# Kernel optimization log

Measured on AMD Instinct MI355X. Metric: run time of the kernel, lower is better.

The kernel has to match this reference:

```python
import jax, jax.numpy as jnp
import numpy as np

K = 7            # kernel size per spatial dim
HALF = K // 2    # 3
WIN = K * K      # 49


def _rel_dist():
    # matches torch: meshgrid('ij') of arange(k)-k//2, euclidean dist, flattened row-major
    c = np.arange(K, dtype=np.float32) - HALF
    gi, gj = np.meshgrid(c, c, indexing='ij')
    return jnp.asarray(np.sqrt(gi ** 2 + gj ** 2).reshape(-1))


def _unfold2d(t):
    B, H, W, C = t.shape
    p = jnp.pad(t, ((0, 0), (HALF, HALF), (HALF, HALF), (0, 0)))
    wins = [p[:, i:i + H, j:j + W, :] for i in range(K) for j in range(K)]
    return jnp.stack(wins, axis=3)


def setup_inputs() -> dict:
    key = jax.random.key(0)
    k1, k2, k3, k4, k5 = jax.random.split(key, 5)
    B, H, W, C = 4, 64, 64, 128
    x = jax.random.normal(k1, (B, H, W, C), dtype=jnp.float32)
    W_qkv = jax.random.normal(k2, (C, 3 * C), dtype=jnp.float32) * (C ** -0.5)
    # width_proj is zero-initialized in the module; use small random values to exercise the soft mask
    W_width = jax.random.normal(k3, (C, 1), dtype=jnp.float32) * 0.02
    b_width = jax.random.normal(k4, (1,), dtype=jnp.float32) * 0.02
    W_out = jax.random.normal(k5, (C, C), dtype=jnp.float32) * (C ** -0.5)
    return {"x": x, "W_qkv": W_qkv, "W_width": W_width, "b_width": b_width, "W_out": W_out}


def reference(x, W_qkv, W_width, b_width, W_out):
    B, H, W, C = x.shape
    L = H * W
    scale = C ** -0.5
    rel_dist = _rel_dist()
    max_dist = rel_dist.max()

    qkv = x @ W_qkv                              # (B,H,W,3C)
    q, k, v = jnp.split(qkv, 3, axis=-1)
    width = jax.nn.sigmoid(x @ W_width + b_width) * max_dist + 0.5  # (B,H,W,1)

    k_win = _unfold2d(k).reshape(B, L, WIN, C)
    v_win = _unfold2d(v).reshape(B, L, WIN, C)
    q_flat = q.reshape(B, L, C)
    width_flat = width.reshape(B, L, 1)

    scores = jnp.einsum('blc,blwc->blw', q_flat, k_win) * scale
    soft_mask = jax.nn.sigmoid((width_flat - rel_dist) * 5.0)
    scores = scores - (1.0 - soft_mask) * 10000.0
    attn = jax.nn.softmax(scores, axis=-1)
    out = jnp.einsum('blw,blwc->blc', attn, v_win).reshape(B, H, W, C)
    return (out + v) @ W_out
```

## Files before the change

### kernel.cpp

```cpp
#include <hip/hip_runtime.h>

#define C 128
#define NPIX 16384
#define THREE_C 384

typedef unsigned short u16;
typedef unsigned int u32;
typedef short bf16x8 __attribute__((ext_vector_type(8)));
typedef float f32x4 __attribute__((ext_vector_type(4)));

__device__ __forceinline__ float bf2f(u16 h) { return __uint_as_float(((u32)h) << 16); }
__device__ __forceinline__ u16 f2bf(float f) {
    u32 b = __float_as_uint(f);
    b += 0x7FFF + ((b >> 16) & 1);
    return (u16)(b >> 16);
}
__device__ __forceinline__ u32 pack2(float a, float b) {
    return (u32)f2bf(a) | ((u32)f2bf(b) << 16);
}

#define GST 136

__global__ __launch_bounds__(256) void qkv_kernel(const float* __restrict__ x,
                                                  const float* __restrict__ Wqkv,
                                                  const float* __restrict__ Wwidth,
                                                  const float* __restrict__ bwidth,
                                                  const float* __restrict__ Wout,
                                                  u16* __restrict__ qb,
                                                  u16* __restrict__ kb,
                                                  u16* __restrict__ vb,
                                                  float* __restrict__ width_g,
                                                  u16* __restrict__ wot) {
    __shared__ u16 xs[64 * GST];
    __shared__ u16 wt[128 * GST];
    const int task = ((int)(blockIdx.x & 7)) * 96 + ((int)blockIdx.x >> 3);
    const int rb = task / 3;
    const int nb = task % 3;
    const int p0 = rb * 64;
    const int tid = threadIdx.x;
    const int wv = tid >> 6;
    const int l = tid & 63;
    const int l15 = l & 15;
    const int l4 = l >> 4;

#pragma unroll
    for (int t = 0; t < 8; ++t) {
        const int f = tid + t * 256;
        const int kq = f & 31, r = f >> 5;
        const float4 xv = *(const float4*)(x + (size_t)(p0 + r) * C + kq * 4);
        uint2 pk;
        pk.x = pack2(xv.x, xv.y);
        pk.y = pack2(xv.z, xv.w);
        *(uint2*)&xs[r * GST + kq * 4] = pk;
    }
#pragma unroll
    for (int t = 0; t < 16; ++t) {
        const int f = tid + t * 256;
        const int c = f & 127, kq = f >> 7;
        const float w0 = Wqkv[(size_t)(kq * 4 + 0) * THREE_C + nb * 128 + c];
        const float w1 = Wqkv[(size_t)(kq * 4 + 1) * THREE_C + nb * 128 + c];
        const float w2 = Wqkv[(size_t)(kq * 4 + 2) * THREE_C + nb * 128 + c];
        const float w3 = Wqkv[(size_t)(kq * 4 + 3) * THREE_C + nb * 128 + c];
        uint2 pk;
        pk.x = pack2(w0, w1);
        pk.y = pack2(w2, w3);
        *(uint2*)&wt[c * GST + kq * 4] = pk;
    }
    if (task < 8) {
        const int base = (task * 256 + tid) * 8;
        const int c = base >> 7, k0 = base & 127;
        uint4 pk;
        pk.x = pack2(Wout[(size_t)(k0 + 0) * C + c], Wout[(size_t)(k0 + 1) * C + c]);
        pk.y = pack2(Wout[(size_t)(k0 + 2) * C + c], Wout[(size_t)(k0 + 3) * C + c]);
        pk.z = pack2(Wout[(size_t)(k0 + 4) * C + c], Wout[(size_t)(k0 + 5) * C + c]);
        pk.w = pack2(Wout[(size_t)(k0 + 6) * C + c], Wout[(size_t)(k0 + 7) * C + c]);
        *(uint4*)&wot[base] = pk;
    }
    __syncthreads();

    if (nb == 0 && tid < 64) {
        float wacc = 0.f;
#pragma unroll
        for (int kk = 0; kk < C; ++kk) wacc += bf2f(xs[tid * GST + kk]) * Wwidth[kk];
        const float z = wacc + bwidth[0];
        width_g[p0 + tid] = (1.f / (1.f + __expf(-z))) * 4.242640687f + 0.5f;
    }

    const int strip = wv * 16;
    bf16x8 af[4];
#pragma unroll
    for (int kf = 0; kf < 4; ++kf)
        af[kf] = *(const bf16x8*)&xs[(strip + l15) * GST + kf * 32 + l4 * 8];

    f32x4 acc[8];
#pragma unroll
    for (int nf = 0; nf < 8; ++nf) acc[nf] = (f32x4){0.f, 0.f, 0.f, 0.f};
#pragma unroll
    for (int nf = 0; nf < 8; ++nf) {
#pragma unroll
        for (int kf = 0; kf < 4; ++kf) {
            const bf16x8 bf = *(const bf16x8*)&wt[(nf * 16 + l15) * GST + kf * 32 + l4 * 8];
            acc[nf] = __builtin_amdgcn_mfma_f32_16x16x32_bf16(af[kf], bf, acc[nf], 0, 0, 0);
        }
    }

    u16* dst = (nb == 0) ? qb : (nb == 1) ? kb : vb;
#pragma unroll
    for (int nf = 0; nf < 8; ++nf) {
        const int col = nf * 16 + l15;
#pragma unroll
        for (int r = 0; r < 4; ++r) {
            const int row = strip + l4 * 4 + r;
            dst[(size_t)(p0 + row) * C + col] = f2bf(acc[nf][r]);
        }
    }
}

#define HSTRIDE 136
#define TSTRIDE 236
#define VSWZ(ch, h) ((h) ^ ((((ch) >> 3) & 3) << 3))

__global__ __launch_bounds__(1024) void attn_kernel(const u16* __restrict__ qb,
                                                    const u16* __restrict__ kb,
                                                    const u16* __restrict__ vb,
                                                    const float* __restrict__ width_g,
                                                    const u16* __restrict__ wot,
                                                    float* __restrict__ out) {
    __shared__ u16 Kl[208 * HSTRIDE];
    __shared__ u16 Vt[128 * TSTRIDE];
    __shared__ u16 Pl[64 * TSTRIDE];
    __shared__ float rsum[4][64];
    __shared__ float wdl[64];

    const int tid = threadIdx.x;
    const int wv = tid >> 6;
    const int l = tid & 63;
    const int l15 = l & 15;
    const int l4 = l >> 4;

    const int W = ((int)blockIdx.x & 7) * 32 + ((int)blockIdx.x >> 3);
    const int b = W >> 6;
    const int t = W & 63;
    const int i0 = (t >> 3) * 8;
    const int j0 = (t & 7) * 8;
    const int pbase = b * 4096;

    if (tid < 64)
        wdl[tid] = width_g[pbase + (i0 + (tid >> 3)) * 64 + j0 + (tid & 7)];

    const uint4 z4 = make_uint4(0, 0, 0, 0);
    uint4 kreg[4];
    int koff[4];
    bool kw[4];
#pragma unroll
    for (int rr = 0; rr < 4; ++rr) {
        const int f = tid + rr * 1024;
        kw[rr] = (f < 3328);
        kreg[rr] = z4;
        const int c = f & 15, h = f >> 4;
        koff[rr] = h * HSTRIDE + c * 8;
        if (kw[rr] && h < 196) {
            const int hi = (h * 2341) >> 15;
            const int hj = h - hi * 14;
            const int ii = i0 - 3 + hi, jj = j0 - 3 + hj;
            if (((unsigned)ii < 64u) && ((unsigned)jj < 64u))
                kreg[rr] = *(const uint4*)(kb + (size_t)(pbase + ii * 64 + jj) * C + c * 8);
        }
    }
    uint4 va[2], vz[2];
    int vc8[2], vh[2];
    bool vw[2];
#pragma unroll
    for (int rr = 0; rr < 2; ++rr) {
        const int f = tid + rr * 1024;
        vw[rr] = (f < 1792);
        va[rr] = z4; vz[rr] = z4;
        const int c8 = f & 15, h = ((f >> 4) * 2) & 255;
        vc8[rr] = c8; vh[rr] = h;
        if (vw[rr]) {
            {
                const int hi = (h * 2341) >> 15;
                const int hj = h - hi * 14;
                const int ii = i0 - 3 + hi, jj = j0 - 3 + hj;
                if ((h < 196) && ((unsigned)ii < 64u) && ((unsigned)jj < 64u))
                    va[rr] = *(const uint4*)(vb + (size_t)(pbase + ii * 64 + jj) * C + c8 * 8);
            }
            {
                const int h1 = h + 1;
                const int hi = (h1 * 2341) >> 15;
                const int hj = h1 - hi * 14;
                const int ii = i0 - 3 + hi, jj = j0 - 3 + hj;
                if ((h1 < 196) && ((unsigned)ii < 64u) && ((unsigned)jj < 64u))
                    vz[rr] = *(const uint4*)(vb + (size_t)(pbase + ii * 64 + jj) * C + c8 * 8);
            }
        }
    }
#pragma unroll
    for (int rr = 0; rr < 4; ++rr)
        if (kw[rr]) *(uint4*)&Kl[koff[rr]] = kreg[rr];
    {
        union { uint4 u4; u16 us[8]; } ua, uz;
        ua.u4 = va[0]; uz.u4 = vz[0];
        const int c8 = vc8[0], h = vh[0];
#pragma unroll
        for (int s = 0; s < 8; ++s) {
            const int ch = c8 * 8 + s;
            *(u32*)&Vt[ch * TSTRIDE + VSWZ(ch, h)] = (u32)ua.us[s] | ((u32)uz.us[s] << 16);
        }
    }

    const int strip = wv >> 2;
    const int g = wv & 3;
    bf16x8 qf[4];
    {
        const int qr = strip * 16 + l15;
        const int p = pbase + (i0 + (qr >> 3)) * 64 + j0 + (qr & 7);
#pragma unroll
        for (int kf = 0; kf < 4; ++kf)
            qf[kf] = *(const bf16x8*)(qb + (size_t)p * C + kf * 32 + l4 * 8);
    }
    __syncthreads();

    f32x4 sv[4];
#pragma unroll
    for (int tt = 0; tt < 4; ++tt) {
        const int nf = g + 4 * tt;
        f32x4 acc = {0.f, 0.f, 0.f, 0.f};
        if (nf < 13) {
            const u16* kr = Kl + (nf * 16 + l15) * HSTRIDE + l4 * 8;
#pragma unroll
            for (int kf = 0; kf < 4; ++kf)
                acc = __builtin_amdgcn_mfma_f32_16x16x32_bf16(
                    qf[kf], *(const bf16x8*)(kr + kf * 32), acc, 0, 0, 0);
        }
        sv[tt] = acc;
    }

    if (vw[1]) {
        union { uint4 u4; u16 us[8]; } ua, uz;
        ua.u4 = va[1]; uz.u4 = vz[1];
        const int c8 = vc8[1], h = vh[1];
#pragma unroll
        for (int s = 0; s < 8; ++s) {
            const int ch = c8 * 8 + s;
            *(u32*)&Vt[ch * TSTRIDE + VSWZ(ch, h)] = (u32)ua.us[s] | ((u32)uz.us[s] << 16);
        }
    }

    uint4 wcopy0 = *(const uint4*)(wot + tid * 8);
    uint4 wcopy1 = *(const uint4*)(wot + (tid + 1024) * 8);

    const int qrb = strip * 16 + l4 * 4;
    float wdr[4];
#pragma unroll
    for (int r = 0; r < 4; ++r) wdr[r] = wdl[qrb + r];
    float smr[4] = {0.f, 0.f, 0.f, 0.f};
#pragma unroll
    for (int tt = 0; tt < 4; ++tt) {
        const int nf = g + 4 * tt;
        if (nf < 13) {
            const int n = nf * 16 + l15;
            const int hi = (n * 2341) >> 15;
            const int hj = n - hi * 14;
#pragma unroll
            for (int r = 0; r < 4; ++r) {
                const int qr = qrb + r;
                const int di = hi - 3 - (qr >> 3);
                const int dj = hj - 3 - (qr & 7);
                const bool valid = ((unsigned)(di + 3) <= 6u) && ((unsigned)(dj + 3) <= 6u);
                float e = 0.f;
                if (valid) {
                    const float rd = sqrtf((float)(di * di + dj * dj));
                    const float sm = 1.f / (1.f + __expf(-5.f * (wdr[r] - rd)));
                    e = __expf(sv[tt][r] * 0.08838834765f - (1.f - sm) * 10000.f);
                }
                sv[tt][r] = e;
                smr[r] += e;
                Pl[qr * TSTRIDE + n] = f2bf(e);
            }
        } else if (nf == 13) {
            const int n = 208 + l15;
#pragma unroll
            for (int r = 0; r < 4; ++r)
                Pl[(qrb + r) * TSTRIDE + n] = 0;
        }
    }
#pragma unroll
    for (int r = 0; r < 4; ++r) {
        float s = smr[r];
        s += __shfl_xor(s, 1);
        s += __shfl_xor(s, 2);
        s += __shfl_xor(s, 4);
        s += __shfl_xor(s, 8);
        smr[r] = s;
    }
    if (l15 == 0) {
#pragma unroll
        for (int r = 0; r < 4; ++r) rsum[g][qrb + r] = smr[r];
    }
    __syncthreads();

    u16* wtl = Kl;
    {
        const int c0 = tid >> 4, k0 = (tid & 15) * 8;
        *(uint4*)&wtl[c0 * GST + k0] = wcopy0;
        const int c1 = 64 + (tid >> 4);
        *(uint4*)&wtl[c1 * GST + k0] = wcopy1;
    }

    float invr[4];
#pragma unroll
    for (int r = 0; r < 4; ++r) {
        const int qr = qrb + r;
        invr[r] = 1.f / (rsum[0][qr] + rsum[1][qr] + rsum[2][qr] + rsum[3][qr]);
    }

    f32x4 oacc[2];
    oacc[0] = (f32x4){0.f, 0.f, 0.f, 0.f};
    oacc[1] = (f32x4){0.f, 0.f, 0.f, 0.f};
#pragma unroll
    for (int kf = 0; kf < 7; ++kf) {
        const bf16x8 pa = *(const bf16x8*)(Pl + (strip * 16 + l15) * TSTRIDE + kf * 32 + l4 * 8);
#pragma unroll
        for (int nf2 = 0; nf2 < 2; ++nf2) {
            const int ch = g * 32 + nf2 * 16 + l15;
            const bf16x8 vf = *(const bf16x8*)(Vt + ch * TSTRIDE + VSWZ(ch, kf * 32 + l4 * 8));
            oacc[nf2] = __builtin_amdgcn_mfma_f32_16x16x32_bf16(pa, vf, oacc[nf2], 0, 0, 0);
        }
    }

    u16* ylds = Kl + 128 * GST;
#pragma unroll
    for (int nf2 = 0; nf2 < 2; ++nf2) {
        const int cch = g * 32 + nf2 * 16 + l15;
#pragma unroll
        for (int r = 0; r < 4; ++r) {
            const int qr = qrb + r;
            const int h = 45 + (qr >> 3) * 14 + (qr & 7);
            const float vv = bf2f(Vt[cch * TSTRIDE + VSWZ(cch, h)]);
            ylds[qr * GST + cch] = f2bf(oacc[nf2][r] * invr[r] + vv);
        }
    }
    __syncthreads();

    bf16x8 yf[4];
#pragma unroll
    for (int kf = 0; kf < 4; ++kf)
        yf[kf] = *(const bf16x8*)&ylds[(strip * 16 + l15) * GST + kf * 32 + l4 * 8];

    f32x4 oc[2];
    oc[0] = (f32x4){0.f, 0.f, 0.f, 0.f};
    oc[1] = (f32x4){0.f, 0.f, 0.f, 0.f};
#pragma unroll
    for (int u = 0; u < 2; ++u) {
        const int nf = g + 4 * u;
#pragma unroll
        for (int kf = 0; kf < 4; ++kf) {
            const bf16x8 bf = *(const bf16x8*)&wtl[(nf * 16 + l15) * GST + kf * 32 + l4 * 8];
            oc[u] = __builtin_amdgcn_mfma_f32_16x16x32_bf16(yf[kf], bf, oc[u], 0, 0, 0);
        }
    }
#pragma unroll
    for (int u = 0; u < 2; ++u) {
        const int col = (g + 4 * u) * 16 + l15;
#pragma unroll
        for (int r = 0; r < 4; ++r) {
            const int qr = qrb + r;
            const int p = pbase + (i0 + (qr >> 3)) * 64 + j0 + (qr & 7);
            out[(size_t)p * C + col] = oc[u][r];
        }
    }
}

extern "C" void kernel_launch(void* const* d_in, const int* in_sizes, int n_in,
                              void* d_out, int out_size, void* d_ws, size_t ws_size,
                              hipStream_t stream) {
    const float* x      = (const float*)d_in[0];
    const float* Wqkv   = (const float*)d_in[1];
    const float* Wwidth = (const float*)d_in[2];
    const float* bwidth = (const float*)d_in[3];
    const float* Wout   = (const float*)d_in[4];
    float* out = (float*)d_out;

    u16* qb = (u16*)d_ws;
    u16* kb = qb + (size_t)NPIX * C;
    u16* vb = kb + (size_t)NPIX * C;
    float* width = (float*)(vb + (size_t)NPIX * C);
    u16* wot = (u16*)(width + NPIX);

    qkv_kernel<<<768, 256, 0, stream>>>(x, Wqkv, Wwidth, bwidth, Wout, qb, kb, vb, width, wot);
    attn_kernel<<<256, 1024, 0, stream>>>(qb, kb, vb, width, wot, out);
}
```

Before: 27.04 us.

## Fuse QKV projection and attention into one cooperative kernel with grid sync

Merges the QKV projection kernel and the attention kernel into a single cooperative launch of 256 blocks of 1024 threads. Each block first projects its own 64 pixels for Q, K and V, then a grid-wide sync is taken before the neighbourhood attention phase. This removes one kernel launch and the gap between the two launches. In exchange, the projection phase runs on only 256 large blocks instead of 768 smaller ones, each block reloads the full weight matrix, and the grid barrier adds its own cost. The old two-kernel path is kept as a fallback if the cooperative launch fails.

```diff
diff --git a/kernel.cpp b/kernel.cpp
--- a/kernel.cpp
+++ b/kernel.cpp
@@ -1,4 +1,7 @@
 #include <hip/hip_runtime.h>
+#include <hip/hip_cooperative_groups.h>
+
+namespace cg = cooperative_groups;
 
 #define C 128
 #define NPIX 16384
@@ -20,125 +23,117 @@
 }
 
 #define GST 136
-
-__global__ __launch_bounds__(256) void qkv_kernel(const float* __restrict__ x,
-                                                  const float* __restrict__ Wqkv,
-                                                  const float* __restrict__ Wwidth,
-                                                  const float* __restrict__ bwidth,
-                                                  const float* __restrict__ Wout,
-                                                  u16* __restrict__ qb,
-                                                  u16* __restrict__ kb,
-                                                  u16* __restrict__ vb,
-                                                  float* __restrict__ width_g,
-                                                  u16* __restrict__ wot) {
-    __shared__ u16 xs[64 * GST];
-    __shared__ u16 wt[128 * GST];
-    const int task = ((int)(blockIdx.x & 7)) * 96 + ((int)blockIdx.x >> 3);
-    const int rb = task / 3;
-    const int nb = task % 3;
-    const int p0 = rb * 64;
+#define HSTRIDE 136
+#define TSTRIDE 236
+#define VSWZ(ch, h) ((h) ^ ((((ch) >> 3) & 3) << 3))
+
+__global__ __launch_bounds__(1024) void fused_kernel(const float* __restrict__ x,
+                                                     const float* __restrict__ Wqkv,
+                                                     const float* __restrict__ Wwidth,
+                                                     const float* __restrict__ bwidth,
+                                                     const float* __restrict__ Wout,
+                                                     u16* __restrict__ qb,
+                                                     u16* __restrict__ kb,
+                                                     u16* __restrict__ vb,
+                                                     float* __restrict__ width_g,
+                                                     u16* __restrict__ wot,
+                                                     float* __restrict__ out) {
+    __shared__ u16 SL[73600];
+    __shared__ float rsum[4][64];
+    __shared__ float wdl[64];
+    u16* Kl = SL;
+    u16* Vt = SL + 28288;
+    u16* Pl = SL + 58496;
+    u16* xs  = SL;
+    u16* wtA = SL + 8704;
+
     const int tid = threadIdx.x;
     const int wv = tid >> 6;
     const int l = tid & 63;
     const int l15 = l & 15;
     const int l4 = l >> 4;
 
-#pragma unroll
-    for (int t = 0; t < 8; ++t) {
-        const int f = tid + t * 256;
-        const int kq = f & 31, r = f >> 5;
-        const float4 xv = *(const float4*)(x + (size_t)(p0 + r) * C + kq * 4);
-        uint2 pk;
-        pk.x = pack2(xv.x, xv.y);
-        pk.y = pack2(xv.z, xv.w);
-        *(uint2*)&xs[r * GST + kq * 4] = pk;
-    }
-#pragma unroll
-    for (int t = 0; t < 16; ++t) {
-        const int f = tid + t * 256;
-        const int c = f & 127, kq = f >> 7;
-        const float w0 = Wqkv[(size_t)(kq * 4 + 0) * THREE_C + nb * 128 + c];
-        const float w1 = Wqkv[(size_t)(kq * 4 + 1) * THREE_C + nb * 128 + c];
-        const float w2 = Wqkv[(size_t)(kq * 4 + 2) * THREE_C + nb * 128 + c];
-        const float w3 = Wqkv[(size_t)(kq * 4 + 3) * THREE_C + nb * 128 + c];
-        uint2 pk;
-        pk.x = pack2(w0, w1);
-        pk.y = pack2(w2, w3);
-        *(uint2*)&wt[c * GST + kq * 4] = pk;
-    }
-    if (task < 8) {
-        const int base = (task * 256 + tid) * 8;
-        const int c = base >> 7, k0 = base & 127;
-        uint4 pk;
-        pk.x = pack2(Wout[(size_t)(k0 + 0) * C + c], Wout[(size_t)(k0 + 1) * C + c]);
-        pk.y = pack2(Wout[(size_t)(k0 + 2) * C + c], Wout[(size_t)(k0 + 3) * C + c]);
-        pk.z = pack2(Wout[(size_t)(k0 + 4) * C + c], Wout[(size_t)(k0 + 5) * C + c]);
-        pk.w = pack2(Wout[(size_t)(k0 + 6) * C + c], Wout[(size_t)(k0 + 7) * C + c]);
-        *(uint4*)&wot[base] = pk;
-    }
-    __syncthreads();
-
-    if (nb == 0 && tid < 64) {
-        float wacc = 0.f;
-#pragma unroll
-        for (int kk = 0; kk < C; ++kk) wacc += bf2f(xs[tid * GST + kk]) * Wwidth[kk];
-        const float z = wacc + bwidth[0];
-        width_g[p0 + tid] = (1.f / (1.f + __expf(-z))) * 4.242640687f + 0.5f;
-    }
-
-    const int strip = wv * 16;
-    bf16x8 af[4];
-#pragma unroll
-    for (int kf = 0; kf < 4; ++kf)
-        af[kf] = *(const bf16x8*)&xs[(strip + l15) * GST + kf * 32 + l4 * 8];
-
-    f32x4 acc[8];
-#pragma unroll
-    for (int nf = 0; nf < 8; ++nf) acc[nf] = (f32x4){0.f, 0.f, 0.f, 0.f};
-#pragma unroll
-    for (int nf = 0; nf < 8; ++nf) {
-#pragma unroll
-        for (int kf = 0; kf < 4; ++kf) {
-            const bf16x8 bf = *(const bf16x8*)&wt[(nf * 16 + l15) * GST + kf * 32 + l4 * 8];
-            acc[nf] = __builtin_amdgcn_mfma_f32_16x16x32_bf16(af[kf], bf, acc[nf], 0, 0, 0);
-        }
-    }
-
-    u16* dst = (nb == 0) ? qb : (nb == 1) ? kb : vb;
-#pragma unroll
-    for (int nf = 0; nf < 8; ++nf) {
-        const int col = nf * 16 + l15;
-#pragma unroll
-        for (int r = 0; r < 4; ++r) {
-            const int row = strip + l4 * 4 + r;
-            dst[(size_t)(p0 + row) * C + col] = f2bf(acc[nf][r]);
-        }
-    }
-}
-
-#define HSTRIDE 136
-#define TSTRIDE 236
-#define VSWZ(ch, h) ((h) ^ ((((ch) >> 3) & 3) << 3))
-
-__global__ __launch_bounds__(1024) void attn_kernel(const u16* __restrict__ qb,
-                                                    const u16* __restrict__ kb,
-                                                    const u16* __restrict__ vb,
-                                                    const float* __restrict__ width_g,
-                                                    const u16* __restrict__ wot,
-                                                    float* __restrict__ out) {
-    __shared__ u16 Kl[208 * HSTRIDE];
-    __shared__ u16 Vt[128 * TSTRIDE];
-    __shared__ u16 Pl[64 * TSTRIDE];
-    __shared__ float rsum[4][64];
-    __shared__ float wdl[64];
-
-    const int tid = threadIdx.x;
-    const int wv = tid >> 6;
-    const int l = tid & 63;
-    const int l15 = l & 15;
-    const int l4 = l >> 4;
-
-    const int W = ((int)blockIdx.x & 7) * 32 + ((int)blockIdx.x >> 3);
+    const int W = ((int)(blockIdx.x & 7) << 5) + ((int)blockIdx.x >> 3);
+
+    {
+        const int p0 = W * 64;
+#pragma unroll
+        for (int t = 0; t < 2; ++t) {
+            const int f = tid + t * 1024;
+            const int kq = f & 31, r = f >> 5;
+            const float4 xv = *(const float4*)(x + (size_t)(p0 + r) * C + kq * 4);
+            uint2 pk;
+            pk.x = pack2(xv.x, xv.y);
+            pk.y = pack2(xv.z, xv.w);
+            *(uint2*)&xs[r * GST + kq * 4] = pk;
+        }
+#pragma unroll
+        for (int nb = 0; nb < 3; ++nb) {
+#pragma unroll
+            for (int t = 0; t < 4; ++t) {
+                const int f = tid + t * 1024;
+                const int c = f & 127, kq = f >> 7;
+                const float w0 = Wqkv[(size_t)(kq * 4 + 0) * THREE_C + nb * 128 + c];
+                const float w1 = Wqkv[(size_t)(kq * 4 + 1) * THREE_C + nb * 128 + c];
+                const float w2 = Wqkv[(size_t)(kq * 4 + 2) * THREE_C + nb * 128 + c];
+                const float w3 = Wqkv[(size_t)(kq * 4 + 3) * THREE_C + nb * 128 + c];
+                uint2 pk;
+                pk.x = pack2(w0, w1);
+                pk.y = pack2(w2, w3);
+                *(uint2*)&wtA[(nb * 128 + c) * GST + kq * 4] = pk;
+            }
+        }
+        if (W < 8 && tid < 256) {
+            const int base = (W * 256 + tid) * 8;
+            const int c = base >> 7, k0 = base & 127;
+            uint4 pk;
+            pk.x = pack2(Wout[(size_t)(k0 + 0) * C + c], Wout[(size_t)(k0 + 1) * C + c]);
+            pk.y = pack2(Wout[(size_t)(k0 + 2) * C + c], Wout[(size_t)(k0 + 3) * C + c]);
+            pk.z = pack2(Wout[(size_t)(k0 + 4) * C + c], Wout[(size_t)(k0 + 5) * C + c]);
+            pk.w = pack2(Wout[(size_t)(k0 + 6) * C + c], Wout[(size_t)(k0 + 7) * C + c]);
+            *(uint4*)&wot[base] = pk;
+        }
+        __syncthreads();
+
+        if (tid < 64) {
+            float wacc = 0.f;
+#pragma unroll
+            for (int kk = 0; kk < C; ++kk) wacc += bf2f(xs[tid * GST + kk]) * Wwidth[kk];
+            const float z = wacc + bwidth[0];
+            width_g[p0 + tid] = (1.f / (1.f + __expf(-z))) * 4.242640687f + 0.5f;
+        }
+
+        const int strip = (wv >> 2) * 16;
+        const int g = wv & 3;
+        bf16x8 af[4];
+#pragma unroll
+        for (int kf = 0; kf < 4; ++kf)
+            af[kf] = *(const bf16x8*)&xs[(strip + l15) * GST + kf * 32 + l4 * 8];
+
+#pragma unroll
+        for (int nb = 0; nb < 3; ++nb) {
+            u16* dst = (nb == 0) ? qb : (nb == 1) ? kb : vb;
+#pragma unroll
+            for (int u = 0; u < 2; ++u) {
+                const int nf = g + 4 * u;
+                f32x4 acc = {0.f, 0.f, 0.f, 0.f};
+#pragma unroll
+                for (int kf = 0; kf < 4; ++kf) {
+                    const bf16x8 bf = *(const bf16x8*)&wtA[(nb * 128 + nf * 16 + l15) * GST + kf * 32 + l4 * 8];
+                    acc = __builtin_amdgcn_mfma_f32_16x16x32_bf16(af[kf], bf, acc, 0, 0, 0);
+                }
+                const int col = nf * 16 + l15;
+#pragma unroll
+                for (int r = 0; r < 4; ++r) {
+                    const int row = strip + l4 * 4 + r;
+                    dst[(size_t)(p0 + row) * C + col] = f2bf(acc[r]);
+                }
+            }
+        }
+    }
+
+    cg::this_grid().sync();
+
     const int b = W >> 6;
     const int t = W & 63;
     const int i0 = (t >> 3) * 8;
@@ -372,6 +367,353 @@
     }
 }
 
+__global__ __launch_bounds__(256) void qkv_kernel(const float* __restrict__ x,
+                                                  const float* __restrict__ Wqkv,
+                                                  const float* __restrict__ Wwidth,
+                                                  const float* __restrict__ bwidth,
+                                                  const float* __restrict__ Wout,
+                                                  u16* __restrict__ qb,
+                                                  u16* __restrict__ kb,
+                                                  u16* __restrict__ vb,
+                                                  float* __restrict__ width_g,
+                                                  u16* __restrict__ wot) {
+    __shared__ u16 xs[64 * GST];
+    __shared__ u16 wt[128 * GST];
+    const int task = ((int)(blockIdx.x & 7)) * 96 + ((int)blockIdx.x >> 3);
+    const int rb = task / 3;
+    const int nb = task % 3;
+    const int p0 = rb * 64;
+    const int tid = threadIdx.x;
+    const int wv = tid >> 6;
+    const int l = tid & 63;
+    const int l15 = l & 15;
+    const int l4 = l >> 4;
+
+#pragma unroll
+    for (int t = 0; t < 8; ++t) {
+        const int f = tid + t * 256;
+        const int kq = f & 31, r = f >> 5;
+        const float4 xv = *(const float4*)(x + (size_t)(p0 + r) * C + kq * 4);
+        uint2 pk;
+        pk.x = pack2(xv.x, xv.y);
+        pk.y = pack2(xv.z, xv.w);
+        *(uint2*)&xs[r * GST + kq * 4] = pk;
+    }
+#pragma unroll
+    for (int t = 0; t < 16; ++t) {
+        const int f = tid + t * 256;
+        const int c = f & 127, kq = f >> 7;
+        const float w0 = Wqkv[(size_t)(kq * 4 + 0) * THREE_C + nb * 128 + c];
+        const float w1 = Wqkv[(size_t)(kq * 4 + 1) * THREE_C + nb * 128 + c];
+        const float w2 = Wqkv[(size_t)(kq * 4 + 2) * THREE_C + nb * 128 + c];
+        const float w3 = Wqkv[(size_t)(kq * 4 + 3) * THREE_C + nb * 128 + c];
+        uint2 pk;
+        pk.x = pack2(w0, w1);
+        pk.y = pack2(w2, w3);
+        *(uint2*)&wt[c * GST + kq * 4] = pk;
+    }
+    if (task < 8) {
+        const int base = (task * 256 + tid) * 8;
+        const int c = base >> 7, k0 = base & 127;
+        uint4 pk;
+        pk.x = pack2(Wout[(size_t)(k0 + 0) * C + c], Wout[(size_t)(k0 + 1) * C + c]);
+        pk.y = pack2(Wout[(size_t)(k0 + 2) * C + c], Wout[(size_t)(k0 + 3) * C + c]);
+        pk.z = pack2(Wout[(size_t)(k0 + 4) * C + c], Wout[(size_t)(k0 + 5) * C + c]);
+        pk.w = pack2(Wout[(size_t)(k0 + 6) * C + c], Wout[(size_t)(k0 + 7) * C + c]);
+        *(uint4*)&wot[base] = pk;
+    }
+    __syncthreads();
+
+    if (nb == 0 && tid < 64) {
+        float wacc = 0.f;
+#pragma unroll
+        for (int kk = 0; kk < C; ++kk) wacc += bf2f(xs[tid * GST + kk]) * Wwidth[kk];
+        const float z = wacc + bwidth[0];
+        width_g[p0 + tid] = (1.f / (1.f + __expf(-z))) * 4.242640687f + 0.5f;
+    }
+
+    const int strip = wv * 16;
+    bf16x8 af[4];
+#pragma unroll
+    for (int kf = 0; kf < 4; ++kf)
+        af[kf] = *(const bf16x8*)&xs[(strip + l15) * GST + kf * 32 + l4 * 8];
+
+    f32x4 acc[8];
+#pragma unroll
+    for (int nf = 0; nf < 8; ++nf) acc[nf] = (f32x4){0.f, 0.f, 0.f, 0.f};
+#pragma unroll
+    for (int nf = 0; nf < 8; ++nf) {
+#pragma unroll
+        for (int kf = 0; kf < 4; ++kf) {
+            const bf16x8 bf = *(const bf16x8*)&wt[(nf * 16 + l15) * GST + kf * 32 + l4 * 8];
+            acc[nf] = __builtin_amdgcn_mfma_f32_16x16x32_bf16(af[kf], bf, acc[nf], 0, 0, 0);
+        }
+    }
+
+    u16* dst = (nb == 0) ? qb : (nb == 1) ? kb : vb;
+#pragma unroll
+    for (int nf = 0; nf < 8; ++nf) {
+        const int col = nf * 16 + l15;
+#pragma unroll
+        for (int r = 0; r < 4; ++r) {
+            const int row = strip + l4 * 4 + r;
+            dst[(size_t)(p0 + row) * C + col] = f2bf(acc[nf][r]);
+        }
+    }
+}
+
+__global__ __launch_bounds__(1024) void attn_kernel(const u16* __restrict__ qb,
+                                                    const u16* __restrict__ kb,
+                                                    const u16* __restrict__ vb,
+                                                    const float* __restrict__ width_g,
+                                                    const u16* __restrict__ wot,
+                                                    float* __restrict__ out) {
+    __shared__ u16 Kl[208 * HSTRIDE];
+    __shared__ u16 Vt[128 * TSTRIDE];
+    __shared__ u16 Pl[64 * TSTRIDE];
+    __shared__ float rsum[4][64];
+    __shared__ float wdl[64];
+
+    const int tid = threadIdx.x;
+    const int wv = tid >> 6;
+    const int l = tid & 63;
+    const int l15 = l & 15;
+    const int l4 = l >> 4;
+
+    const int W = ((int)blockIdx.x & 7) * 32 + ((int)blockIdx.x >> 3);
+    const int b = W >> 6;
+    const int t = W & 63;
+    const int i0 = (t >> 3) * 8;
+    const int j0 = (t & 7) * 8;
+    const int pbase = b * 4096;
+
+    if (tid < 64)
+        wdl[tid] = width_g[pbase + (i0 + (tid >> 3)) * 64 + j0 + (tid & 7)];
+
+    const uint4 z4 = make_uint4(0, 0, 0, 0);
+    uint4 kreg[4];
+    int koff[4];
+    bool kw[4];
+#pragma unroll
+    for (int rr = 0; rr < 4; ++rr) {
+        const int f = tid + rr * 1024;
+        kw[rr] = (f < 3328);
+        kreg[rr] = z4;
+        const int c = f & 15, h = f >> 4;
+        koff[rr] = h * HSTRIDE + c * 8;
+        if (kw[rr] && h < 196) {
+            const int hi = (h * 2341) >> 15;
+            const int hj = h - hi * 14;
+            const int ii = i0 - 3 + hi, jj = j0 - 3 + hj;
+            if (((unsigned)ii < 64u) && ((unsigned)jj < 64u))
+                kreg[rr] = *(const uint4*)(kb + (size_t)(pbase + ii * 64 + jj) * C + c * 8);
+        }
+    }
+    uint4 va[2], vz[2];
+    int vc8[2], vh[2];
+    bool vw[2];
+#pragma unroll
+    for (int rr = 0; rr < 2; ++rr) {
+        const int f = tid + rr * 1024;
+        vw[rr] = (f < 1792);
+        va[rr] = z4; vz[rr] = z4;
+        const int c8 = f & 15, h = ((f >> 4) * 2) & 255;
+        vc8[rr] = c8; vh[rr] = h;
+        if (vw[rr]) {
+            {
+                const int hi = (h * 2341) >> 15;
+                const int hj = h - hi * 14;
+                const int ii = i0 - 3 + hi, jj = j0 - 3 + hj;
+                if ((h < 196) && ((unsigned)ii < 64u) && ((unsigned)jj < 64u))
+                    va[rr] = *(const uint4*)(vb + (size_t)(pbase + ii * 64 + jj) * C + c8 * 8);
+            }
+            {
+                const int h1 = h + 1;
+                const int hi = (h1 * 2341) >> 15;
+                const int hj = h1 - hi * 14;
+                const int ii = i0 - 3 + hi, jj = j0 - 3 + hj;
+                if ((h1 < 196) && ((unsigned)ii < 64u) && ((unsigned)jj < 64u))
+                    vz[rr] = *(const uint4*)(vb + (size_t)(pbase + ii * 64 + jj) * C + c8 * 8);
+            }
+        }
+    }
+#pragma unroll
+    for (int rr = 0; rr < 4; ++rr)
+        if (kw[rr]) *(uint4*)&Kl[koff[rr]] = kreg[rr];
+    {
+        union { uint4 u4; u16 us[8]; } ua, uz;
+        ua.u4 = va[0]; uz.u4 = vz[0];
+        const int c8 = vc8[0], h = vh[0];
+#pragma unroll
+        for (int s = 0; s < 8; ++s) {
+            const int ch = c8 * 8 + s;
+            *(u32*)&Vt[ch * TSTRIDE + VSWZ(ch, h)] = (u32)ua.us[s] | ((u32)uz.us[s] << 16);
+        }
+    }
+
+    const int strip = wv >> 2;
+    const int g = wv & 3;
+    bf16x8 qf[4];
+    {
+        const int qr = strip * 16 + l15;
+        const int p = pbase + (i0 + (qr >> 3)) * 64 + j0 + (qr & 7);
+#pragma unroll
+        for (int kf = 0; kf < 4; ++kf)
+            qf[kf] = *(const bf16x8*)(qb + (size_t)p * C + kf * 32 + l4 * 8);
+    }
+    __syncthreads();
+
+    f32x4 sv[4];
+#pragma unroll
+    for (int tt = 0; tt < 4; ++tt) {
+        const int nf = g + 4 * tt;
+        f32x4 acc = {0.f, 0.f, 0.f, 0.f};
+        if (nf < 13) {
+            const u16* kr = Kl + (nf * 16 + l15) * HSTRIDE + l4 * 8;
+#pragma unroll
+            for (int kf = 0; kf < 4; ++kf)
+                acc = __builtin_amdgcn_mfma_f32_16x16x32_bf16(
+                    qf[kf], *(const bf16x8*)(kr + kf * 32), acc, 0, 0, 0);
+        }
+        sv[tt] = acc;
+    }
+
+    if (vw[1]) {
+        union { uint4 u4; u16 us[8]; } ua, uz;
+        ua.u4 = va[1]; uz.u4 = vz[1];
+        const int c8 = vc8[1], h = vh[1];
+#pragma unroll
+        for (int s = 0; s < 8; ++s) {
+            const int ch = c8 * 8 + s;
+            *(u32*)&Vt[ch * TSTRIDE + VSWZ(ch, h)] = (u32)ua.us[s] | ((u32)uz.us[s] << 16);
+        }
+    }
+
+    uint4 wcopy0 = *(const uint4*)(wot + tid * 8);
+    uint4 wcopy1 = *(const uint4*)(wot + (tid + 1024) * 8);
+
+    const int qrb = strip * 16 + l4 * 4;
+    float wdr[4];
+#pragma unroll
+    for (int r = 0; r < 4; ++r) wdr[r] = wdl[qrb + r];
+    float smr[4] = {0.f, 0.f, 0.f, 0.f};
+#pragma unroll
+    for (int tt = 0; tt < 4; ++tt) {
+        const int nf = g + 4 * tt;
+        if (nf < 13) {
+            const int n = nf * 16 + l15;
+            const int hi = (n * 2341) >> 15;
+            const int hj = n - hi * 14;
+#pragma unroll
+            for (int r = 0; r < 4; ++r) {
+                const int qr = qrb + r;
+                const int di = hi - 3 - (qr >> 3);
+                const int dj = hj - 3 - (qr & 7);
+                const bool valid = ((unsigned)(di + 3) <= 6u) && ((unsigned)(dj + 3) <= 6u);
+                float e = 0.f;
+                if (valid) {
+                    const float rd = sqrtf((float)(di * di + dj * dj));
+                    const float sm = 1.f / (1.f + __expf(-5.f * (wdr[r] - rd)));
+                    e = __expf(sv[tt][r] * 0.08838834765f - (1.f - sm) * 10000.f);
+                }
+                sv[tt][r] = e;
+                smr[r] += e;
+                Pl[qr * TSTRIDE + n] = f2bf(e);
+            }
+        } else if (nf == 13) {
+            const int n = 208 + l15;
+#pragma unroll
+            for (int r = 0; r < 4; ++r)
+                Pl[(qrb + r) * TSTRIDE + n] = 0;
+        }
+    }
+#pragma unroll
+    for (int r = 0; r < 4; ++r) {
+        float s = smr[r];
+        s += __shfl_xor(s, 1);
+        s += __shfl_xor(s, 2);
+        s += __shfl_xor(s, 4);
+        s += __shfl_xor(s, 8);
+        smr[r] = s;
+    }
+    if (l15 == 0) {
+#pragma unroll
+        for (int r = 0; r < 4; ++r) rsum[g][qrb + r] = smr[r];
+    }
+    __syncthreads();
+
+    u16* wtl = Kl;
+    {
+        const int c0 = tid >> 4, k0 = (tid & 15) * 8;
+        *(uint4*)&wtl[c0 * GST + k0] = wcopy0;
+        const int c1 = 64 + (tid >> 4);
+        *(uint4*)&wtl[c1 * GST + k0] = wcopy1;
+    }
+
+    float invr[4];
+#pragma unroll
+    for (int r = 0; r < 4; ++r) {
+        const int qr = qrb + r;
+        invr[r] = 1.f / (rsum[0][qr] + rsum[1][qr] + rsum[2][qr] + rsum[3][qr]);
+    }
+
+    f32x4 oacc[2];
+    oacc[0] = (f32x4){0.f, 0.f, 0.f, 0.f};
+    oacc[1] = (f32x4){0.f, 0.f, 0.f, 0.f};
+#pragma unroll
+    for (int kf = 0; kf < 7; ++kf) {
+        const bf16x8 pa = *(const bf16x8*)(Pl + (strip * 16 + l15) * TSTRIDE + kf * 32 + l4 * 8);
+#pragma unroll
+        for (int nf2 = 0; nf2 < 2; ++nf2) {
+            const int ch = g * 32 + nf2 * 16 + l15;
+            const bf16x8 vf = *(const bf16x8*)(Vt + ch * TSTRIDE + VSWZ(ch, kf * 32 + l4 * 8));
+            oacc[nf2] = __builtin_amdgcn_mfma_f32_16x16x32_bf16(pa, vf, oacc[nf2], 0, 0, 0);
+        }
+    }
+
+    u16* ylds = Kl + 128 * GST;
+#pragma unroll
+    for (int nf2 = 0; nf2 < 2; ++nf2) {
+        const int cch = g * 32 + nf2 * 16 + l15;
+#pragma unroll
+        for (int r = 0; r < 4; ++r) {
+            const int qr = qrb + r;
+            const int h = 45 + (qr >> 3) * 14 + (qr & 7);
+            const float vv = bf2f(Vt[cch * TSTRIDE + VSWZ(cch, h)]);
+            ylds[qr * GST + cch] = f2bf(oacc[nf2][r] * invr[r] + vv);
+        }
+    }
+    __syncthreads();
+
+    bf16x8 yf[4];
+#pragma unroll
+    for (int kf = 0; kf < 4; ++kf)
+        yf[kf] = *(const bf16x8*)&ylds[(strip * 16 + l15) * GST + kf * 32 + l4 * 8];
+
+    f32x4 oc[2];
+    oc[0] = (f32x4){0.f, 0.f, 0.f, 0.f};
+    oc[1] = (f32x4){0.f, 0.f, 0.f, 0.f};
+#pragma unroll
+    for (int u = 0; u < 2; ++u) {
+        const int nf = g + 4 * u;
+#pragma unroll
+        for (int kf = 0; kf < 4; ++kf) {
+            const bf16x8 bf = *(const bf16x8*)&wtl[(nf * 16 + l15) * GST + kf * 32 + l4 * 8];
+            oc[u] = __builtin_amdgcn_mfma_f32_16x16x32_bf16(yf[kf], bf, oc[u], 0, 0, 0);
+        }
+    }
+#pragma unroll
+    for (int u = 0; u < 2; ++u) {
+        const int col = (g + 4 * u) * 16 + l15;
+#pragma unroll
+        for (int r = 0; r < 4; ++r) {
+            const int qr = qrb + r;
+            const int p = pbase + (i0 + (qr >> 3)) * 64 + j0 + (qr & 7);
+            out[(size_t)p * C + col] = oc[u][r];
+        }
+    }
+}
+
 extern "C" void kernel_launch(void* const* d_in, const int* in_sizes, int n_in,
                               void* d_out, int out_size, void* d_ws, size_t ws_size,
                               hipStream_t stream) {
@@ -388,6 +730,12 @@
     float* width = (float*)(vb + (size_t)NPIX * C);
     u16* wot = (u16*)(width + NPIX);
 
-    qkv_kernel<<<768, 256, 0, stream>>>(x, Wqkv, Wwidth, bwidth, Wout, qb, kb, vb, width, wot);
-    attn_kernel<<<256, 1024, 0, stream>>>(qb, kb, vb, width, wot, out);
+    void* args[] = {(void*)&x, (void*)&Wqkv, (void*)&Wwidth, (void*)&bwidth, (void*)&Wout,
+                    (void*)&qb, (void*)&kb, (void*)&vb, (void*)&width, (void*)&wot, (void*)&out};
+    hipError_t err = hipLaunchCooperativeKernel((void*)fused_kernel, dim3(256), dim3(1024),
+                                                args, 0, stream);
+    if (err != hipSuccess) {
+        qkv_kernel<<<768, 256, 0, stream>>>(x, Wqkv, Wwidth, bwidth, Wout, qb, kb, vb, width, wot);
+        attn_kernel<<<256, 1024, 0, stream>>>(qb, kb, vb, width, wot, out);
+    }
 }
```

Result: slower. 77.40 us (+186.2%).
